# Kernel optimization log

Hardware: AMD Instinct MI355X
Metric: run time of the kernel (lower is better)

Reference implementation:

```python
import jax, jax.numpy as jnp
import numpy as np

WINDOW_SIZE = 8
NUM_HEADS = 16
KAN_GRID = 5
GRID_MIN, GRID_MAX = -2.0, 2.0


def _relative_position_index(ws: int) -> np.ndarray:
    # Same construction as the Keras __init__: pairwise 2D relative coords -> flat index
    coords = np.stack(np.meshgrid(np.arange(ws), np.arange(ws), indexing='ij'))  # [2,ws,ws]
    flat = coords.reshape(2, -1)                                                 # [2,N]
    rel = flat[:, :, None] - flat[:, None, :]                                    # [2,N,N]
    rel = rel.transpose(1, 2, 0)                                                 # [N,N,2]
    rh = (rel[:, :, 0] + ws - 1) * (2 * ws - 1)
    rw = rel[:, :, 1] + ws - 1
    return (rh + rw).astype(np.int32)                                            # [N,N]

_REL_IDX = _relative_position_index(WINDOW_SIZE)


def setup_inputs() -> dict:
    key = jax.random.key(0)
    ks = jax.random.split(key, 8)
    B, N, C = 512, WINDOW_SIZE * WINDOW_SIZE, 512
    G = KAN_GRID
    s = 0.02
    return {
        'x': jax.random.normal(ks[0], (B, N, C), jnp.float32),
        'Wq': jax.random.normal(ks[1], (C, C), jnp.float32) * s,
        'Wk_base': jax.random.normal(ks[2], (C, C), jnp.float32) * s,
        'Wk_spline': jax.random.normal(ks[3], (C * G, C), jnp.float32) * s,
        'Wv': jax.random.normal(ks[4], (C, C), jnp.float32) * s,
        'Wproj': jax.random.normal(ks[5], (C, C), jnp.float32) * s,
        'bproj': jnp.zeros((C,), jnp.float32),
        'bias_table': jax.random.normal(ks[6], ((2 * WINDOW_SIZE - 1) ** 2, NUM_HEADS), jnp.float32) * s,
    }


def _kan_key(x, W_base, W_spline):
    # FastKAN-style KANLinear: base path = swish(x) @ W_base,
    # spline path = Gaussian-RBF basis over each input channel, linearly combined.
    B, N, C = x.shape
    G = KAN_GRID
    grid = jnp.linspace(GRID_MIN, GRID_MAX, G).astype(x.dtype)          # [G]
    h = (GRID_MAX - GRID_MIN) / (G - 1)
    phi = jnp.exp(-(((x[..., None] - grid) / h) ** 2))                  # [B,N,C,G]
    spline = phi.reshape(B, N, C * G) @ W_spline                        # [B,N,C]
    base = jax.nn.swish(x) @ W_base                                     # [B,N,C]
    return base + spline


def reference(x, Wq, Wk_base, Wk_spline, Wv, Wproj, bproj, bias_table):
    B, N, C = x.shape
    H = NUM_HEADS
    hd = C // H
    scale = hd ** -0.5

    def split_heads(t):  # [B,N,C] -> [B,H,N,hd]
        return t.reshape(B, N, H, hd).transpose(0, 2, 1, 3)

    q = split_heads(x @ Wq)
    k = split_heads(_kan_key(x, Wk_base, Wk_spline))
    v = split_heads(x @ Wv)

    scores = jnp.einsum('bhnd,bhmd->bhnm', q, k) * scale                # [B,H,N,N]
    bias = bias_table[_REL_IDX]                                         # [N,N,H]
    scores = scores + bias.transpose(2, 0, 1)[None]                     # + [1,H,N,N]
    # internal padding mask: input already fills the full window, mask is all-ones -> no-op,
    # kept structurally: mask==0 positions would be set to large negative before softmax.
    attn = jax.nn.softmax(scores, axis=-1)
    ctx = jnp.einsum('bhnm,bhmd->bhnd', attn, v)                        # [B,H,N,hd]
    ctx = ctx.transpose(0, 2, 1, 3).reshape(B, N, C)
    return ctx @ Wproj + bproj
```

## Files before the change

kernel.cpp:

```cpp
#include <hip/hip_runtime.h>
#include <hip/hip_bf16.h>

using bf16 = __bf16;
typedef __bf16 bf16x8 __attribute__((ext_vector_type(8)));
typedef float  f32x4  __attribute__((ext_vector_type(4)));

__global__ void prep(const float* __restrict__ x, bf16* __restrict__ xb,
                     bf16* __restrict__ swb, int n)
{
    int base = (blockIdx.x * 256 + threadIdx.x) * 8;
    if (base >= n) return;
    float4 a = *(const float4*)(x + base);
    float4 b = *(const float4*)(x + base + 4);
    float xs[8] = {a.x, a.y, a.z, a.w, b.x, b.y, b.z, b.w};
    bf16x8 xo, so;
#pragma unroll
    for (int t = 0; t < 8; ++t) {
        xo[t] = (bf16)xs[t];
        so[t] = (bf16)(xs[t] / (1.0f + __expf(-xs[t])));
    }
    *(bf16x8*)(xb  + base) = xo;
    *(bf16x8*)(swb + base) = so;
}

__global__ void transpose_k(const float* __restrict__ W, bf16* __restrict__ Wt,
                            int K, int N, int ldT, int total)
{
    int idx = blockIdx.x * 256 + threadIdx.x;
    if (idx >= total) return;
    int k = idx % K;
    int n = idx / K;
    Wt[(size_t)n * ldT + k] = (bf16)W[(size_t)k * N + n];
}

template<int AMODE, bool BIAS, typename CT>
__global__ __launch_bounds__(512, 4)
void gemm_bt(const bf16* __restrict__ A, const float* __restrict__ X,
             const bf16* __restrict__ Bt, CT* __restrict__ C,
             int M, int K, const float* __restrict__ bias)
{
    constexpr int LDA = 40;
    __shared__ bf16 As[64 * LDA];
    __shared__ bf16 Bs[512 * LDA];

    const int tid  = threadIdx.x;
    const int lane = tid & 63;
    const int wave = tid >> 6;
    const int quad = lane >> 4;
    const int l15  = lane & 15;
    const int m0   = blockIdx.x * 64;

    f32x4 acc[4][4] = {};

    for (int kt = 0; kt < K; kt += 32) {
#pragma unroll
        for (int cc = 0; cc < 4; ++cc) {
            const int chunk = cc * 512 + tid;
            const int row   = chunk >> 2;
            const int col8  = (chunk & 3) * 8;
            *(bf16x8*)(Bs + row * LDA + col8) =
                *(const bf16x8*)(Bt + (size_t)row * K + kt + col8);
        }
        if (tid < 256) {
            const int row  = tid >> 2;
            const int col8 = (tid & 3) * 8;
            if (AMODE == 0) {
                *(bf16x8*)(As + row * LDA + col8) =
                    *(const bf16x8*)(A + (size_t)(m0 + row) * K + kt + col8);
            } else {
                const int kg = kt + col8;
                if (kg < 512) {
                    *(bf16x8*)(As + row * LDA + col8) =
                        *(const bf16x8*)(A + (size_t)(m0 + row) * 512 + kg);
                } else {
                    const int ks = kg - 512;
                    const int c0 = ks / 5;
                    const int r0 = ks - c0 * 5;
                    const float* xr = X + (size_t)(m0 + row) * 512 + c0;
                    const float x0 = xr[0];
                    const float x1 = xr[1];
                    const float x2v = xr[(c0 < 510) ? 2 : 1];
                    bf16x8 o;
                    float xv = x0, xnext = x1;
                    int g = r0;
#pragma unroll
                    for (int t = 0; t < 8; ++t) {
                        float d = xv - (float)(g - 2);
                        o[t] = (bf16)__expf(-d * d);
                        if (++g == 5) { g = 0; xv = xnext; xnext = x2v; }
                    }
                    *(bf16x8*)(As + row * LDA + col8) = o;
                }
            }
        }
        __syncthreads();

        bf16x8 af[4], bfr[4];
#pragma unroll
        for (int i = 0; i < 4; ++i)
            af[i] = *(const bf16x8*)(As + (i * 16 + l15) * LDA + quad * 8);
#pragma unroll
        for (int j = 0; j < 4; ++j)
            bfr[j] = *(const bf16x8*)(Bs + (wave * 64 + j * 16 + l15) * LDA + quad * 8);
#pragma unroll
        for (int i = 0; i < 4; ++i)
#pragma unroll
            for (int j = 0; j < 4; ++j)
                acc[i][j] = __builtin_amdgcn_mfma_f32_16x16x32_bf16(af[i], bfr[j], acc[i][j], 0, 0, 0);
        __syncthreads();
    }

#pragma unroll
    for (int i = 0; i < 4; ++i) {
#pragma unroll
        for (int j = 0; j < 4; ++j) {
            const int col = wave * 64 + j * 16 + l15;
            const float bv = BIAS ? bias[col] : 0.0f;
#pragma unroll
            for (int r = 0; r < 4; ++r) {
                const int row = m0 + i * 16 + quad * 4 + r;
                C[(size_t)row * 512 + col] = (CT)(acc[i][j][r] + bv);
            }
        }
    }
}

__global__ __launch_bounds__(256)
void attn_mfma(const bf16* __restrict__ q, const bf16* __restrict__ k,
               const bf16* __restrict__ v, const float* __restrict__ bias_table,
               bf16* __restrict__ ctx)
{
    constexpr int LQ = 40;
    constexpr int LV = 72;
    __shared__ bf16 qs[64 * LQ];
    __shared__ bf16 ks[64 * LQ];
    __shared__ bf16 vsT[32 * LV];
    __shared__ bf16 Pl[4][16 * LV];
    __shared__ float bl[225];

    const int bid  = blockIdx.x;
    const int b    = bid >> 4;
    const int h    = bid & 15;
    const int tid  = threadIdx.x;
    const int lane = tid & 63;
    const int w    = tid >> 6;
    const int quad = lane >> 4;
    const int l15  = lane & 15;

    const int n  = tid >> 2;
    const int d0 = (tid & 3) * 8;
    const size_t gbase = ((size_t)(b * 64 + n)) * 512 + h * 32 + d0;
    {
        bf16x8 rq = *(const bf16x8*)(q + gbase);
        bf16x8 rk = *(const bf16x8*)(k + gbase);
        bf16x8 rv = *(const bf16x8*)(v + gbase);
        *(bf16x8*)(qs + n * LQ + d0) = rq;
        *(bf16x8*)(ks + n * LQ + d0) = rk;
#pragma unroll
        for (int t = 0; t < 8; ++t) vsT[(d0 + t) * LV + n] = rv[t];
    }
    if (tid < 225) bl[tid] = bias_table[tid * 16 + h];
    __syncthreads();

    f32x4 sacc[4] = {};
    {
        bf16x8 aq = *(const bf16x8*)(qs + (w * 16 + l15) * LQ + quad * 8);
#pragma unroll
        for (int j = 0; j < 4; ++j) {
            bf16x8 bk = *(const bf16x8*)(ks + (j * 16 + l15) * LQ + quad * 8);
            sacc[j] = __builtin_amdgcn_mfma_f32_16x16x32_bf16(aq, bk, sacc[j], 0, 0, 0);
        }
    }

    bf16* Pw = Pl[w];
    float inv[4];
    {
        const float scale = 0.17677669529663687f;
#pragma unroll
        for (int r = 0; r < 4; ++r) {
            const int row = w * 16 + quad * 4 + r;
            const int rh = row >> 3, rw = row & 7;
            float pv[4];
            float mx = -1e30f;
#pragma unroll
            for (int j = 0; j < 4; ++j) {
                const int c   = j * 16 + l15;
                const int idx = (rh - (c >> 3) + 7) * 15 + (rw - (c & 7) + 7);
                float s = sacc[j][r] * scale + bl[idx];
                pv[j] = s;
                mx = fmaxf(mx, s);
            }
            mx = fmaxf(mx, __shfl_xor(mx, 1, 64));
            mx = fmaxf(mx, __shfl_xor(mx, 2, 64));
            mx = fmaxf(mx, __shfl_xor(mx, 4, 64));
            mx = fmaxf(mx, __shfl_xor(mx, 8, 64));
            float sum = 0.0f;
#pragma unroll
            for (int j = 0; j < 4; ++j) {
                float e = __expf(pv[j] - mx);
                pv[j] = e;
                sum += e;
            }
            sum += __shfl_xor(sum, 1, 64);
            sum += __shfl_xor(sum, 2, 64);
            sum += __shfl_xor(sum, 4, 64);
            sum += __shfl_xor(sum, 8, 64);
            inv[r] = 1.0f / sum;
#pragma unroll
            for (int j = 0; j < 4; ++j)
                Pw[(quad * 4 + r) * LV + j * 16 + l15] = (bf16)pv[j];
        }
    }

    f32x4 oacc[2] = {};
#pragma unroll
    for (int mc = 0; mc < 2; ++mc) {
        bf16x8 ap = *(const bf16x8*)(Pw + l15 * LV + mc * 32 + quad * 8);
#pragma unroll
        for (int dt = 0; dt < 2; ++dt) {
            bf16x8 bv = *(const bf16x8*)(vsT + (dt * 16 + l15) * LV + mc * 32 + quad * 8);
            oacc[dt] = __builtin_amdgcn_mfma_f32_16x16x32_bf16(ap, bv, oacc[dt], 0, 0, 0);
        }
    }

#pragma unroll
    for (int dt = 0; dt < 2; ++dt)
#pragma unroll
        for (int r = 0; r < 4; ++r)
            qs[(w * 16 + quad * 4 + r) * LQ + dt * 16 + l15] = (bf16)(oacc[dt][r] * inv[r]);

    bf16x8 ov = *(const bf16x8*)(qs + n * LQ + d0);
    *(bf16x8*)(ctx + gbase) = ov;
}

extern "C" void kernel_launch(void* const* d_in, const int* in_sizes, int n_in,
                              void* d_out, int out_size, void* d_ws, size_t ws_size,
                              hipStream_t stream)
{
    const float* x       = (const float*)d_in[0];
    const float* Wq      = (const float*)d_in[1];
    const float* Wk_base = (const float*)d_in[2];
    const float* Wk_spl  = (const float*)d_in[3];
    const float* Wv      = (const float*)d_in[4];
    const float* Wproj   = (const float*)d_in[5];
    const float* bproj   = (const float*)d_in[6];
    const float* btab    = (const float*)d_in[7];

    bf16* ws  = (bf16*)d_ws;
    bf16* wqT = ws;
    bf16* wvT = ws + 262144;
    bf16* wpT = ws + 524288;
    bf16* wkT = ws + 786432;
    bf16* xb  = ws + 2359296;
    bf16* q   = ws + 19136512;
    bf16* kk  = ws + 35913728;
    bf16* swb = (bf16*)d_out;
    bf16* vv  = (bf16*)d_out + 16777216;
    bf16* ctx = q;

    prep<<<8192, 256, 0, stream>>>(x, xb, swb, 16777216);

    transpose_k<<<1024, 256, 0, stream>>>(Wq,      wqT,       512,  512, 512,  262144);
    transpose_k<<<1024, 256, 0, stream>>>(Wv,      wvT,       512,  512, 512,  262144);
    transpose_k<<<1024, 256, 0, stream>>>(Wproj,   wpT,       512,  512, 512,  262144);
    transpose_k<<<1024, 256, 0, stream>>>(Wk_base, wkT,       512,  512, 3072, 262144);
    transpose_k<<<5120, 256, 0, stream>>>(Wk_spl,  wkT + 512, 2560, 512, 3072, 1310720);

    gemm_bt<0, false, bf16><<<512, 512, 0, stream>>>(xb,  nullptr, wqT, q,  32768, 512,  nullptr);
    gemm_bt<2, false, bf16><<<512, 512, 0, stream>>>(swb, x,       wkT, kk, 32768, 3072, nullptr);
    gemm_bt<0, false, bf16><<<512, 512, 0, stream>>>(xb,  nullptr, wvT, vv, 32768, 512,  nullptr);

    attn_mfma<<<8192, 256, 0, stream>>>(q, kk, vv, btab, ctx);

    gemm_bt<0, true, float><<<512, 512, 0, stream>>>(ctx, nullptr, wpT, (float*)d_out, 32768, 512, bproj);
}
```

Measured before the change: 460.1 us.

## Load B fragments directly from global and double-buffer A tile in LDS

The GEMM no longer stages the 512-row B tile through shared memory. Each wave now loads its B MFMA fragments straight from global memory into registers. The A tile is double-buffered in LDS, which removes the second barrier per k-step, and all 512 threads now share the A load (4 elements each instead of 8 on half the threads). The aim is to cut LDS traffic, barriers and LDS footprint, at the cost of uncoalesced, cache-dependent global reads of B. The occupancy hint drops from 4 to 3 blocks.

```diff
diff --git a/kernel.cpp b/kernel.cpp
--- a/kernel.cpp
+++ b/kernel.cpp
@@ -3,6 +3,7 @@
 
 using bf16 = __bf16;
 typedef __bf16 bf16x8 __attribute__((ext_vector_type(8)));
+typedef __bf16 bf16x4 __attribute__((ext_vector_type(4)));
 typedef float  f32x4  __attribute__((ext_vector_type(4)));
 
 __global__ void prep(const float* __restrict__ x, bf16* __restrict__ xb,
@@ -34,14 +35,13 @@
 }
 
 template<int AMODE, bool BIAS, typename CT>
-__global__ __launch_bounds__(512, 4)
+__global__ __launch_bounds__(512, 3)
 void gemm_bt(const bf16* __restrict__ A, const float* __restrict__ X,
              const bf16* __restrict__ Bt, CT* __restrict__ C,
              int M, int K, const float* __restrict__ bias)
 {
     constexpr int LDA = 40;
-    __shared__ bf16 As[64 * LDA];
-    __shared__ bf16 Bs[512 * LDA];
+    __shared__ bf16 As[2][64 * LDA];
 
     const int tid  = threadIdx.x;
     const int lane = tid & 63;
@@ -50,64 +50,56 @@
     const int l15  = lane & 15;
     const int m0   = blockIdx.x * 64;
 
+    const int srow = tid >> 3;
+    const int scol = (tid & 7) * 4;
+
     f32x4 acc[4][4] = {};
 
-    for (int kt = 0; kt < K; kt += 32) {
-#pragma unroll
-        for (int cc = 0; cc < 4; ++cc) {
-            const int chunk = cc * 512 + tid;
-            const int row   = chunk >> 2;
-            const int col8  = (chunk & 3) * 8;
-            *(bf16x8*)(Bs + row * LDA + col8) =
-                *(const bf16x8*)(Bt + (size_t)row * K + kt + col8);
-        }
-        if (tid < 256) {
-            const int row  = tid >> 2;
-            const int col8 = (tid & 3) * 8;
+    int buf = 0;
+    for (int kt = 0; kt < K; kt += 32, buf ^= 1) {
+        bf16x8 bfr[4];
+#pragma unroll
+        for (int j = 0; j < 4; ++j)
+            bfr[j] = *(const bf16x8*)(Bt + (size_t)(wave * 64 + j * 16 + l15) * K + kt + quad * 8);
+
+        {
+            const int kg = kt + scol;
             if (AMODE == 0) {
-                *(bf16x8*)(As + row * LDA + col8) =
-                    *(const bf16x8*)(A + (size_t)(m0 + row) * K + kt + col8);
+                *(bf16x4*)(As[buf] + srow * LDA + scol) =
+                    *(const bf16x4*)(A + (size_t)(m0 + srow) * K + kg);
+            } else if (kg < 512) {
+                *(bf16x4*)(As[buf] + srow * LDA + scol) =
+                    *(const bf16x4*)(A + (size_t)(m0 + srow) * 512 + kg);
             } else {
-                const int kg = kt + col8;
-                if (kg < 512) {
-                    *(bf16x8*)(As + row * LDA + col8) =
-                        *(const bf16x8*)(A + (size_t)(m0 + row) * 512 + kg);
-                } else {
-                    const int ks = kg - 512;
-                    const int c0 = ks / 5;
-                    const int r0 = ks - c0 * 5;
-                    const float* xr = X + (size_t)(m0 + row) * 512 + c0;
-                    const float x0 = xr[0];
-                    const float x1 = xr[1];
-                    const float x2v = xr[(c0 < 510) ? 2 : 1];
-                    bf16x8 o;
-                    float xv = x0, xnext = x1;
-                    int g = r0;
-#pragma unroll
-                    for (int t = 0; t < 8; ++t) {
-                        float d = xv - (float)(g - 2);
-                        o[t] = (bf16)__expf(-d * d);
-                        if (++g == 5) { g = 0; xv = xnext; xnext = x2v; }
-                    }
-                    *(bf16x8*)(As + row * LDA + col8) = o;
+                const int ks = kg - 512;
+                const int c0 = ks / 5;
+                const int r0 = ks - c0 * 5;
+                const float* xr = X + (size_t)(m0 + srow) * 512 + c0;
+                const float x0 = xr[0];
+                const float x1 = xr[(c0 < 511) ? 1 : 0];
+                bf16x4 o;
+                float xv = x0;
+                int g = r0;
+#pragma unroll
+                for (int t = 0; t < 4; ++t) {
+                    float d = xv - (float)(g - 2);
+                    o[t] = (bf16)__expf(-d * d);
+                    if (++g == 5) { g = 0; xv = x1; }
                 }
+                *(bf16x4*)(As[buf] + srow * LDA + scol) = o;
             }
         }
         __syncthreads();
 
-        bf16x8 af[4], bfr[4];
+        bf16x8 af[4];
 #pragma unroll
         for (int i = 0; i < 4; ++i)
-            af[i] = *(const bf16x8*)(As + (i * 16 + l15) * LDA + quad * 8);
-#pragma unroll
-        for (int j = 0; j < 4; ++j)
-            bfr[j] = *(const bf16x8*)(Bs + (wave * 64 + j * 16 + l15) * LDA + quad * 8);
+            af[i] = *(const bf16x8*)(As[buf] + (i * 16 + l15) * LDA + quad * 8);
 #pragma unroll
         for (int i = 0; i < 4; ++i)
 #pragma unroll
             for (int j = 0; j < 4; ++j)
                 acc[i][j] = __builtin_amdgcn_mfma_f32_16x16x32_bf16(af[i], bfr[j], acc[i][j], 0, 0, 0);
-        __syncthreads();
     }
 
 #pragma unroll
```

New measurement: 508.6 us. 10.5% more time.

## Restructure GEMM with double-buffered A tiles, register-resident B, and 2-way N split

Applied to the files above, without the earlier changes.

The GEMM kernel now uses 256-thread blocks that each compute a 64x256 output tile, so the grid doubles to 1024 blocks. Block IDs are remapped so that groups of eight consecutive blocks are spread across the M range. The K step grows to 64. A tiles are double-buffered in LDS, with global loads and the spline RBF evaluation for the next tile overlapped with MFMA work on the current one. B fragments are loaded straight from global memory into registers, skipping LDS staging, and one barrier per K step is removed. The cost is higher register pressure and B reads that are less coalesced and duplicated per wave.

```diff
diff --git a/kernel.cpp b/kernel.cpp
--- a/kernel.cpp
+++ b/kernel.cpp
@@ -3,6 +3,7 @@
 
 using bf16 = __bf16;
 typedef __bf16 bf16x8 __attribute__((ext_vector_type(8)));
+typedef __bf16 bf16x4 __attribute__((ext_vector_type(4)));
 typedef float  f32x4  __attribute__((ext_vector_type(4)));
 
 __global__ void prep(const float* __restrict__ x, bf16* __restrict__ xb,
@@ -34,87 +35,125 @@
 }
 
 template<int AMODE, bool BIAS, typename CT>
-__global__ __launch_bounds__(512, 4)
+__global__ __launch_bounds__(256, 2)
 void gemm_bt(const bf16* __restrict__ A, const float* __restrict__ X,
              const bf16* __restrict__ Bt, CT* __restrict__ C,
              int M, int K, const float* __restrict__ bias)
 {
-    constexpr int LDA = 40;
-    __shared__ bf16 As[64 * LDA];
-    __shared__ bf16 Bs[512 * LDA];
+    constexpr int LDA = 72;
+    __shared__ bf16 As[2][64 * LDA];
+
+    const int nwg = gridDim.x;
+    const int bid = ((int)blockIdx.x & 7) * (nwg >> 3) + ((int)blockIdx.x >> 3);
 
     const int tid  = threadIdx.x;
     const int lane = tid & 63;
     const int wave = tid >> 6;
     const int quad = lane >> 4;
     const int l15  = lane & 15;
-    const int m0   = blockIdx.x * 64;
-
+    const int m0   = (bid >> 1) * 64;
+    const int n0   = (bid & 1) * 256;
+
+    struct ARaw { bf16x8 d[2]; float x[2][3]; };
     f32x4 acc[4][4] = {};
 
-    for (int kt = 0; kt < K; kt += 32) {
-#pragma unroll
-        for (int cc = 0; cc < 4; ++cc) {
-            const int chunk = cc * 512 + tid;
-            const int row   = chunk >> 2;
-            const int col8  = (chunk & 3) * 8;
-            *(bf16x8*)(Bs + row * LDA + col8) =
-                *(const bf16x8*)(Bt + (size_t)row * K + kt + col8);
-        }
-        if (tid < 256) {
-            const int row  = tid >> 2;
-            const int col8 = (tid & 3) * 8;
+    auto load_raw = [&](int kt, ARaw& r) {
+#pragma unroll
+        for (int cc = 0; cc < 2; ++cc) {
+            const int chunk = cc * 256 + tid;
+            const int row   = chunk >> 3;
+            const int col8  = (chunk & 7) * 8;
+            const int kg = kt + col8;
             if (AMODE == 0) {
-                *(bf16x8*)(As + row * LDA + col8) =
-                    *(const bf16x8*)(A + (size_t)(m0 + row) * K + kt + col8);
+                r.d[cc] = *(const bf16x8*)(A + (size_t)(m0 + row) * K + kg);
+            } else if (kg < 512) {
+                r.d[cc] = *(const bf16x8*)(A + (size_t)(m0 + row) * 512 + kg);
             } else {
-                const int kg = kt + col8;
-                if (kg < 512) {
-                    *(bf16x8*)(As + row * LDA + col8) =
-                        *(const bf16x8*)(A + (size_t)(m0 + row) * 512 + kg);
-                } else {
-                    const int ks = kg - 512;
-                    const int c0 = ks / 5;
-                    const int r0 = ks - c0 * 5;
-                    const float* xr = X + (size_t)(m0 + row) * 512 + c0;
-                    const float x0 = xr[0];
-                    const float x1 = xr[1];
-                    const float x2v = xr[(c0 < 510) ? 2 : 1];
-                    bf16x8 o;
-                    float xv = x0, xnext = x1;
-                    int g = r0;
-#pragma unroll
-                    for (int t = 0; t < 8; ++t) {
-                        float d = xv - (float)(g - 2);
-                        o[t] = (bf16)__expf(-d * d);
-                        if (++g == 5) { g = 0; xv = xnext; xnext = x2v; }
-                    }
-                    *(bf16x8*)(As + row * LDA + col8) = o;
+                const int ks = kg - 512;
+                const int c0 = ks / 5;
+                const float* xr = X + (size_t)(m0 + row) * 512 + c0;
+                r.x[cc][0] = xr[0];
+                r.x[cc][1] = xr[1];
+                r.x[cc][2] = xr[(c0 < 510) ? 2 : 1];
+            }
+        }
+    };
+    auto store_a = [&](bf16* dst, const ARaw& r, int kt) {
+#pragma unroll
+        for (int cc = 0; cc < 2; ++cc) {
+            const int chunk = cc * 256 + tid;
+            const int row   = chunk >> 3;
+            const int col8  = (chunk & 7) * 8;
+            const int kg = kt + col8;
+            bf16x8 o;
+            if (AMODE == 0 || kg < 512) {
+                o = r.d[cc];
+            } else {
+                const int ks = kg - 512;
+                const int c0 = ks / 5;
+                const int r0 = ks - c0 * 5;
+                float xv = r.x[cc][0], xn = r.x[cc][1], x2 = r.x[cc][2];
+                int g = r0;
+#pragma unroll
+                for (int t = 0; t < 8; ++t) {
+                    float d = xv - (float)(g - 2);
+                    o[t] = (bf16)__expf(-d * d);
+                    if (++g == 5) { g = 0; xv = xn; xn = x2; }
                 }
             }
-        }
+            *(bf16x8*)(dst + row * LDA + col8) = o;
+        }
+    };
+    auto load_b = [&](int kt, bf16x8* f) {
+#pragma unroll
+        for (int h = 0; h < 2; ++h)
+#pragma unroll
+            for (int j = 0; j < 4; ++j)
+                f[h * 4 + j] = *(const bf16x8*)(
+                    Bt + (size_t)(n0 + wave * 64 + j * 16 + l15) * K + kt + h * 32 + quad * 8);
+    };
+    auto compute = [&](const bf16* as, const bf16x8* f) {
+#pragma unroll
+        for (int h = 0; h < 2; ++h)
+#pragma unroll
+            for (int i = 0; i < 4; ++i) {
+                bf16x8 af = *(const bf16x8*)(as + (i * 16 + l15) * LDA + h * 32 + quad * 8);
+#pragma unroll
+                for (int j = 0; j < 4; ++j)
+                    acc[i][j] = __builtin_amdgcn_mfma_f32_16x16x32_bf16(af, f[h * 4 + j], acc[i][j], 0, 0, 0);
+            }
+    };
+
+    const int NT = K >> 6;
+    ARaw ra, rb;
+    bf16x8 fa[8], fb[8];
+
+    load_raw(0, ra);
+    load_b(0, fa);
+    store_a(As[0], ra, 0);
+    load_raw(64, rb);
+    load_b(64, fb);
+    __syncthreads();
+
+    for (int p = 0; p < NT; p += 2) {
+        const int kt = p << 6;
+        compute(As[0], fa);
+        store_a(As[1], rb, kt + 64);
+        if (p + 2 < NT) { load_raw(kt + 128, ra); load_b(kt + 128, fa); }
         __syncthreads();
-
-        bf16x8 af[4], bfr[4];
-#pragma unroll
-        for (int i = 0; i < 4; ++i)
-            af[i] = *(const bf16x8*)(As + (i * 16 + l15) * LDA + quad * 8);
-#pragma unroll
-        for (int j = 0; j < 4; ++j)
-            bfr[j] = *(const bf16x8*)(Bs + (wave * 64 + j * 16 + l15) * LDA + quad * 8);
-#pragma unroll
-        for (int i = 0; i < 4; ++i)
-#pragma unroll
-            for (int j = 0; j < 4; ++j)
-                acc[i][j] = __builtin_amdgcn_mfma_f32_16x16x32_bf16(af[i], bfr[j], acc[i][j], 0, 0, 0);
-        __syncthreads();
+        compute(As[1], fb);
+        if (p + 2 < NT) {
+            store_a(As[0], ra, kt + 128);
+            if (p + 3 < NT) { load_raw(kt + 192, rb); load_b(kt + 192, fb); }
+            __syncthreads();
+        }
     }
 
 #pragma unroll
     for (int i = 0; i < 4; ++i) {
 #pragma unroll
         for (int j = 0; j < 4; ++j) {
-            const int col = wave * 64 + j * 16 + l15;
+            const int col = n0 + wave * 64 + j * 16 + l15;
             const float bv = BIAS ? bias[col] : 0.0f;
 #pragma unroll
             for (int r = 0; r < 4; ++r) {
@@ -266,11 +305,11 @@
     transpose_k<<<1024, 256, 0, stream>>>(Wk_base, wkT,       512,  512, 3072, 262144);
     transpose_k<<<5120, 256, 0, stream>>>(Wk_spl,  wkT + 512, 2560, 512, 3072, 1310720);
 
-    gemm_bt<0, false, bf16><<<512, 512, 0, stream>>>(xb,  nullptr, wqT, q,  32768, 512,  nullptr);
-    gemm_bt<2, false, bf16><<<512, 512, 0, stream>>>(swb, x,       wkT, kk, 32768, 3072, nullptr);
-    gemm_bt<0, false, bf16><<<512, 512, 0, stream>>>(xb,  nullptr, wvT, vv, 32768, 512,  nullptr);
+    gemm_bt<0, false, bf16><<<1024, 256, 0, stream>>>(xb,  nullptr, wqT, q,  32768, 512,  nullptr);
+    gemm_bt<2, false, bf16><<<1024, 256, 0, stream>>>(swb, x,       wkT, kk, 32768, 3072, nullptr);
+    gemm_bt<0, false, bf16><<<1024, 256, 0, stream>>>(xb,  nullptr, wvT, vv, 32768, 512,  nullptr);
 
     attn_mfma<<<8192, 256, 0, stream>>>(q, kk, vv, btab, ctx);
 
-    gemm_bt<0, true, float><<<512, 512, 0, stream>>>(ctx, nullptr, wpT, (float*)d_out, 32768, 512, bproj);
-}
+    gemm_bt<0, true, float><<<1024, 256, 0, stream>>>(ctx, nullptr, wpT, (float*)d_out, 32768, 512, bproj);
+}
```

Result: slower. 512.2 us (+11.3%).
